# Optimization experiments

Measured on AMD Instinct MI355X. Metric: run time of the kernel, lower is better.

## Reference

```python
import jax, jax.numpy as jnp
import numpy as np

N_NODES = 100000
N_EDGES = 1600000
D_FEAT = 128


def setup_inputs() -> dict:
    key = jax.random.key(0)
    k1, k2, k3, k4 = jax.random.split(key, 4)
    support = jax.random.normal(k1, (N_NODES, D_FEAT), dtype=jnp.float32)
    vals = jax.random.uniform(k2, (N_EDGES,), dtype=jnp.float32)
    rows = jax.random.randint(k3, (N_EDGES,), 0, N_NODES, dtype=jnp.int64)
    cols = jax.random.randint(k4, (N_EDGES,), 0, N_NODES, dtype=jnp.int64)
    return {"support": support, "vals": vals, "rows": rows, "cols": cols}


def reference(support, vals, rows, cols):
    # out = adj @ support, adj given in COO: adj[rows[e], cols[e]] = vals[e]
    # Gather neighbor features, scale by edge weight, scatter-add to row nodes.
    msgs = vals[:, None] * support[cols]          # [E, F]
    out = jax.ops.segment_sum(msgs, rows, num_segments=support.shape[0])  # [N, F]
    return out
```

## Files before the change

### kernel.cpp

```cpp
#include <hip/hip_runtime.h>
#include <hip/hip_bf16.h>
#include <hip/hip_fp16.h>


#define D_FEAT 128
#define F4 32
#define H4 32
#define H8 16
#define STRIDE 64
#define OVF_CAP 131072
#define EPT 8
#define BINT 512
#define CAP 4096
#define GMAXIT 8
#define BROWS 200
#define GT 512

typedef float    vfloat4 __attribute__((ext_vector_type(4)));
typedef _Float16 half4v  __attribute__((ext_vector_type(4)));
typedef _Float16 half8v  __attribute__((ext_vector_type(8)));


__global__ __launch_bounds__(BINT) void
phase1_bin_kernel(const float4* __restrict__ support4,
                  half8v* __restrict__ supporth,
                  const int* __restrict__ rows,
                  const int* __restrict__ cols,
                  const float* __restrict__ vals,
                  int2* __restrict__ dense,
                  int* __restrict__ gcur,
                  int4* __restrict__ ovf,
                  int* __restrict__ ovf_count,
                  int E, int BT, int NBLK, int n8) {
    int b = blockIdx.x;
    int tid = threadIdx.x;

    if (b >= NBLK) {
        int m = (b - NBLK) * BINT + tid;
        if (m < n8) {
            float4 a0 = support4[(size_t)m * 2];
            float4 a1 = support4[(size_t)m * 2 + 1];
            half8v h;
            h[0] = (_Float16)a0.x; h[1] = (_Float16)a0.y;
            h[2] = (_Float16)a0.z; h[3] = (_Float16)a0.w;
            h[4] = (_Float16)a1.x; h[5] = (_Float16)a1.y;
            h[6] = (_Float16)a1.z; h[7] = (_Float16)a1.w;
            supporth[m] = h;
        }
        return;
    }

    __shared__ int  hist[512];
    __shared__ int  off[513];
    __shared__ int  sstart[512];
    __shared__ int2 sorted[BINT * EPT];

    for (int i = tid; i < 512; i += BINT) hist[i] = 0;
    __syncthreads();

    int t = b * BINT + tid;
    int   r[EPT];
    int   c[EPT];
    float v[EPT];
    int   rk[EPT];

    #pragma unroll
    for (int i = 0; i < EPT; ++i) {
        int e = t + i * BT;
        r[i] = (e < E) ? rows[e] : -1;
    }
    #pragma unroll
    for (int i = 0; i < EPT; ++i) {
        int e = t + i * BT;
        if (e < E) { c[i] = cols[e]; v[i] = vals[e]; }
    }
    #pragma unroll
    for (int i = 0; i < EPT; ++i)
        rk[i] = (r[i] >= 0) ? atomicAdd(&hist[r[i] / BROWS], 1) : 0;
    __syncthreads();

    if (tid < 64) {
        int l[8];
        int s = 0;
        #pragma unroll
        for (int k = 0; k < 8; ++k) {
            l[k] = hist[tid * 8 + k];
            s += l[k];
        }
        int inc = s;
        #pragma unroll
        for (int dd = 1; dd < 64; dd <<= 1) {
            int tt = __shfl_up(inc, dd, 64);
            if (tid >= dd) inc += tt;
        }
        int run = inc - s;
        #pragma unroll
        for (int k = 0; k < 8; ++k) {
            off[tid * 8 + k] = run;
            run += l[k];
        }
        if (tid == 63) off[512] = run;
    }
    __syncthreads();

    #pragma unroll
    for (int i = 0; i < EPT; ++i) {
        if (r[i] < 0) continue;
        int d = r[i] / BROWS;
        int2 q;
        q.x = ((r[i] - d * BROWS) << 17) | c[i];
        q.y = __float_as_int(v[i]);
        sorted[off[d] + rk[i]] = q;
    }
    __syncthreads();

    {
        int l = off[tid + 1] - off[tid];
        sstart[tid] = (l > 0) ? atomicAdd(&gcur[tid], l) : 0;
    }
    __syncthreads();

    {
        int grp  = tid >> 4;
        int lane = tid & 15;
        for (int d = grp; d < 512; d += 32) {
            int o  = off[d];
            int l  = off[d + 1] - o;
            int st = sstart[d];
            for (int k = lane; k < l; k += 16) {
                int pos = st + k;
                int2 q = sorted[o + k];
                if (pos < CAP) {
                    dense[(size_t)d * CAP + pos] = q;
                } else {
                    int ox = atomicAdd(ovf_count, 1);
                    if (ox < OVF_CAP) {
                        int4 e4;
                        e4.x = d * BROWS + ((q.x >> 17) & 255);
                        e4.y = q.x & 0x1FFFF;
                        e4.z = q.y;
                        e4.w = 0;
                        ovf[ox] = e4;
                    }
                }
            }
        }
    }
}


__global__ __launch_bounds__(GT) void
bucket_csr_gather_kernel(const half8v* __restrict__ supporth,
                         const int2* __restrict__ dense,
                         const int* __restrict__ gcur,
                         float4* __restrict__ out4, int N) {
    __shared__ int  cnt[257];
    __shared__ int  off[257];
    __shared__ int2 csr[CAP + 8];

    const int d   = blockIdx.x;
    const int tid = threadIdx.x;
    const int2* dbase = dense + (size_t)d * CAP;

    int total = gcur[d];
    if (total > CAP) total = CAP;

    if (tid < 257) cnt[tid] = 0;
    __syncthreads();

    int2 ent[GMAXIT];
    int  err[GMAXIT];
    int  ernk[GMAXIT];
    #pragma unroll
    for (int it = 0; it < GMAXIT; ++it) {
        int s = tid + it * GT;
        err[it] = -1;
        if (s < total) {
            int2 q = dbase[s];
            int r = (q.x >> 17) & 255;
            ent[it].x = q.x & 0x1FFFF;
            ent[it].y = q.y;
            err[it] = r;
            ernk[it] = atomicAdd(&cnt[r], 1);
        }
    }
    __syncthreads();

    if (tid < 64) {
        int4 c4 = ((int4*)cnt)[tid];
        int t0 = c4.x;
        int t1 = t0 + c4.y;
        int t2 = t1 + c4.z;
        int t3 = t2 + c4.w;
        int inc = t3;
        #pragma unroll
        for (int dd = 1; dd < 64; dd <<= 1) {
            int t = __shfl_up(inc, dd, 64);
            if (tid >= dd) inc += t;
        }
        int excl = inc - t3;
        off[tid * 4 + 0] = excl;
        off[tid * 4 + 1] = excl + t0;
        off[tid * 4 + 2] = excl + t1;
        off[tid * 4 + 3] = excl + t2;
        if (tid == 63) off[256] = inc;
    }
    __syncthreads();

    #pragma unroll
    for (int it = 0; it < GMAXIT; ++it) {
        if (err[it] >= 0)
            csr[off[err[it]] + ernk[it]] = ent[it];
    }
    __syncthreads();

    const int g = tid >> 4;
    const int i = tid & 15;
    const int base = d * BROWS;
    for (int rq = 0; rq < 7; ++rq) {
        int r = rq * 32 + g;
        if (r >= BROWS) continue;
        int beg = off[r];
        int end = off[r + 1];
        vfloat4 a00 = {0.f,0.f,0.f,0.f}, a01 = {0.f,0.f,0.f,0.f};
        vfloat4 a10 = {0.f,0.f,0.f,0.f}, a11 = {0.f,0.f,0.f,0.f};
        for (int k0 = beg; k0 < end; k0 += 8) {
            int   cc[8];
            float vv[8];
            #pragma unroll
            for (int u = 0; u < 8; ++u) {
                int2 e = csr[k0 + u];
                bool ib = (k0 + u) < end;
                cc[u] = ib ? e.x : 0;
                vv[u] = ib ? __int_as_float(e.y) : 0.f;
            }
            half8v s[8];
            #pragma unroll
            for (int u = 0; u < 8; ++u)
                s[u] = supporth[(size_t)cc[u] * H8 + i];
            #pragma unroll
            for (int u = 0; u < 8; ++u) {
                float v = vv[u];
                if (u & 1) {
                    a10.x += v * (float)s[u][0];
                    a10.y += v * (float)s[u][1];
                    a10.z += v * (float)s[u][2];
                    a10.w += v * (float)s[u][3];
                    a11.x += v * (float)s[u][4];
                    a11.y += v * (float)s[u][5];
                    a11.z += v * (float)s[u][6];
                    a11.w += v * (float)s[u][7];
                } else {
                    a00.x += v * (float)s[u][0];
                    a00.y += v * (float)s[u][1];
                    a00.z += v * (float)s[u][2];
                    a00.w += v * (float)s[u][3];
                    a01.x += v * (float)s[u][4];
                    a01.y += v * (float)s[u][5];
                    a01.z += v * (float)s[u][6];
                    a01.w += v * (float)s[u][7];
                }
            }
        }
        int row = base + r;
        if (row < N) {
            vfloat4 r0, r1;
            r0.x = a00.x + a10.x; r0.y = a00.y + a10.y;
            r0.z = a00.z + a10.z; r0.w = a00.w + a10.w;
            r1.x = a01.x + a11.x; r1.y = a01.y + a11.y;
            r1.z = a01.z + a11.z; r1.w = a01.w + a11.w;
            float4* dst = &out4[(size_t)row * F4 + (i << 1)];
            __builtin_nontemporal_store(r0, (vfloat4*)dst);
            __builtin_nontemporal_store(r1, (vfloat4*)(dst + 1));
        }
    }
}


__global__ void ovf_scatter_kernel(const float* __restrict__ support,
                                   const int4* __restrict__ ovf,
                                   const int* __restrict__ ovf_count,
                                   float* __restrict__ out, int cap) {
    int gid = blockIdx.x * blockDim.x + threadIdx.x;
    int i = gid >> 5;
    int j = gid & 31;
    int istride = (gridDim.x * blockDim.x) >> 5;
    int cnt = *ovf_count;
    if (cnt > cap) cnt = cap;
    for (; i < cnt; i += istride) {
        int4 q = ovf[i];
        float v = __int_as_float(q.z);
        const float4* s4 = (const float4*)support + (size_t)q.y * F4 + j;
        float4 s = *s4;
        float* o = out + (size_t)q.x * D_FEAT + j * 4;
        unsafeAtomicAdd(o + 0, v * s.x);
        unsafeAtomicAdd(o + 1, v * s.y);
        unsafeAtomicAdd(o + 2, v * s.z);
        unsafeAtomicAdd(o + 3, v * s.w);
    }
}


__global__ void convert_kernel(const float4* __restrict__ in,
                               half8v* __restrict__ out, int n8) {
    int t = blockIdx.x * blockDim.x + threadIdx.x;
    if (t >= n8) return;
    float4 a = in[(size_t)t * 2];
    float4 b = in[(size_t)t * 2 + 1];
    half8v h;
    h[0] = (_Float16)a.x; h[1] = (_Float16)a.y;
    h[2] = (_Float16)a.z; h[3] = (_Float16)a.w;
    h[4] = (_Float16)b.x; h[5] = (_Float16)b.y;
    h[6] = (_Float16)b.z; h[7] = (_Float16)b.w;
    out[t] = h;
}

__global__ void gather_half_kernel(const half4v* __restrict__ supporth,
                                   const int* __restrict__ cursor,
                                   const int2* __restrict__ pairs,
                                   float4* __restrict__ out4, int n_nodes) {
    unsigned int t = blockIdx.x * blockDim.x + threadIdx.x;
    unsigned int row = t >> 5;
    unsigned int j = t & 31;
    if (row >= (unsigned int)n_nodes) return;
    int deg = cursor[row];
    if (deg > STRIDE) deg = STRIDE;
    const int2* pr = pairs + (size_t)row * STRIDE;
    int2 z = {0, 0};
    int2 p0 = ((int)j < deg) ? pr[j] : z;
    int2 p1 = ((int)(j + 32) < deg) ? pr[j + 32] : z;
    int   c0 = p0.x;  float v0 = __int_as_float(p0.y);
    int   c1 = p1.x;  float v1 = __int_as_float(p1.y);
    int degr = (deg + 7) & ~7;
    float4 acc[4];
    #pragma unroll
    for (int u = 0; u < 4; ++u) acc[u] = {0.f, 0.f, 0.f, 0.f};
    for (int k = 0; k < degr; k += 8) {
        int   cc[8];
        float vv[8];
        #pragma unroll
        for (int u = 0; u < 8; ++u) {
            int kk = k + u;
            cc[u] = __shfl(kk < 32 ? c0 : c1, kk & 31, 32);
            vv[u] = __shfl(kk < 32 ? v0 : v1, kk & 31, 32);
        }
        half4v s[8];
        #pragma unroll
        for (int u = 0; u < 8; ++u)
            s[u] = supporth[(size_t)cc[u] * H4 + j];
        #pragma unroll
        for (int u = 0; u < 8; ++u) {
            acc[u & 3].x += vv[u] * (float)s[u][0];
            acc[u & 3].y += vv[u] * (float)s[u][1];
            acc[u & 3].z += vv[u] * (float)s[u][2];
            acc[u & 3].w += vv[u] * (float)s[u][3];
        }
    }
    vfloat4 res;
    res.x = (acc[0].x + acc[1].x) + (acc[2].x + acc[3].x);
    res.y = (acc[0].y + acc[1].y) + (acc[2].y + acc[3].y);
    res.z = (acc[0].z + acc[1].z) + (acc[2].z + acc[3].z);
    res.w = (acc[0].w + acc[1].w) + (acc[2].w + acc[3].w);
    __builtin_nontemporal_store(res, (vfloat4*)&out4[(size_t)row * F4 + j]);
}

__global__ void bucket_ilp_kernel(const int* __restrict__ rows,
                                  const int* __restrict__ cols,
                                  const float* __restrict__ vals,
                                  int* __restrict__ cursor,
                                  int* __restrict__ ovf_count,
                                  int2* __restrict__ pairs,
                                  int4* __restrict__ ovf,
                                  int n_edges, int gstride) {
    int tid = blockIdx.x * blockDim.x + threadIdx.x;
    int   r[EPT];
    int   c[EPT];
    float v[EPT];
    int   slot[EPT];
    #pragma unroll
    for (int i = 0; i < EPT; ++i) {
        int e = tid + i * gstride;
        r[i] = (e < n_edges) ? rows[e] : -1;
    }
    #pragma unroll
    for (int i = 0; i < EPT; ++i) {
        int e = tid + i * gstride;
        if (e < n_edges) { c[i] = cols[e]; v[i] = vals[e]; }
    }
    #pragma unroll
    for (int i = 0; i < EPT; ++i)
        slot[i] = (r[i] >= 0) ? atomicAdd(&cursor[r[i]], 1) : 0;
    #pragma unroll
    for (int i = 0; i < EPT; ++i) {
        if (r[i] < 0) continue;
        int2 p;
        p.x = c[i];
        p.y = __float_as_int(v[i]);
        if (slot[i] < STRIDE) {
            pairs[(size_t)r[i] * STRIDE + slot[i]] = p;
        } else {
            int o = atomicAdd(ovf_count, 1);
            if (o < OVF_CAP) {
                int4 q; q.x = r[i]; q.y = p.x; q.z = p.y; q.w = 0;
                ovf[o] = q;
            }
        }
    }
}


__global__ void gc_scatter_kernel(const float* __restrict__ support,
                                  const float* __restrict__ vals,
                                  const int* __restrict__ rows,
                                  const int* __restrict__ cols,
                                  float* __restrict__ out, int n_edges) {
    unsigned int t = blockIdx.x * blockDim.x + threadIdx.x;
    unsigned int e = t >> 5;
    unsigned int j = t & 31;
    if (e >= (unsigned int)n_edges) return;
    int r = rows[e];
    int c = cols[e];
    float v = vals[e];
    const float4* s4 = reinterpret_cast<const float4*>(support) + (size_t)c * F4 + j;
    float4 s = *s4;
    float* o = out + (size_t)r * D_FEAT + j * 4;
    unsafeAtomicAdd(o + 0, v * s.x);
    unsafeAtomicAdd(o + 1, v * s.y);
    unsafeAtomicAdd(o + 2, v * s.z);
    unsafeAtomicAdd(o + 3, v * s.w);
}


extern "C" void kernel_launch(void* const* d_in, const int* in_sizes, int n_in,
                              void* d_out, int out_size, void* d_ws, size_t ws_size,
                              hipStream_t stream) {
    const float* support = (const float*)d_in[0];
    const float* vals    = (const float*)d_in[1];
    const int*   rows    = (const int*)d_in[2];
    const int*   cols    = (const int*)d_in[3];
    float* out = (float*)d_out;

    int E = in_sizes[1];
    int N = in_sizes[0] / D_FEAT;
    int n8 = N * D_FEAT / 8;
    int ND = (N + BROWS - 1) / BROWS;
    int NBLK = (E + BINT * EPT - 1) / (BINT * EPT);
    int BT = NBLK * BINT;

    char* ws = (char*)d_ws;
    size_t cur = 0;
    auto carve = [&](size_t bytes) -> void* {
        void* p = ws + cur;
        cur += (bytes + 255) & ~(size_t)255;
        return p;
    };

    {
        size_t save = cur;
        int2*   dense     = (int2*)carve((size_t)512 * CAP * 8);
        int*    gcur      = (int*)carve((size_t)768 * 4);
        int4*   ovf       = (int4*)carve((size_t)OVF_CAP * 16);
        half8v* supporth  = (half8v*)carve((size_t)N * D_FEAT * 2);
        if (cur <= ws_size && ND <= 512) {
            int* ovf_count = gcur + 512;
            (void)hipMemsetAsync(gcur, 0, (size_t)513 * 4, stream);
            int cblocks = (n8 + BINT - 1) / BINT;
            phase1_bin_kernel<<<NBLK + cblocks, BINT, 0, stream>>>(
                (const float4*)support, supporth, rows, cols, vals,
                dense, gcur, ovf, ovf_count, E, BT, NBLK, n8);
            bucket_csr_gather_kernel<<<ND, GT, 0, stream>>>(
                supporth, dense, gcur, (float4*)out, N);
            ovf_scatter_kernel<<<128, 256, 0, stream>>>(
                support, ovf, ovf_count, out, OVF_CAP);
            return;
        }
        cur = save;
    }

    {
        size_t save = cur;
        int*    cursor   = (int*)carve((size_t)(N + 1) * 4);
        int2*   pairs    = (int2*)carve((size_t)N * STRIDE * 8);
        int4*   ovf      = (int4*)carve((size_t)8192 * 16);
        half8v* supporth = (half8v*)carve((size_t)N * D_FEAT * 2);
        if (cur <= ws_size) {
            int* ovf_count = cursor + N;
            int bthreads = (E + EPT - 1) / EPT;
            int bblocks = (bthreads + 255) / 256;
            int gstride = bblocks * 256;
            (void)hipMemsetAsync(cursor, 0, (size_t)(N + 1) * 4, stream);
            convert_kernel<<<(n8 + 255) / 256, 256, 0, stream>>>(
                (const float4*)support, supporth, n8);
            bucket_ilp_kernel<<<bblocks, 256, 0, stream>>>(
                rows, cols, vals, cursor, ovf_count, pairs, ovf, E, gstride);
            unsigned int gthreads = (unsigned int)N * 32;
            gather_half_kernel<<<(gthreads + 255) / 256, 256, 0, stream>>>(
                (const half4v*)supporth, cursor, pairs, (float4*)out, N);
            ovf_scatter_kernel<<<512, 256, 0, stream>>>(
                support, ovf, ovf_count, out, 8192);
            return;
        }
        cur = save;
    }

    (void)hipMemsetAsync(d_out, 0, (size_t)out_size * sizeof(float), stream);
    unsigned int total = (unsigned int)E * 32;
    gc_scatter_kernel<<<(total + 255) / 256, 256, 0, stream>>>(
        support, vals, rows, cols, out, E);
}
```

Measured before the change: 185.0 us.

## Use finer row buckets and fold overflow edges into bucket gather kernel

Halves rows per bucket (100) and doubles bucket count to 1024, with 1024-thread binning blocks and a smaller per-bucket capacity, so the gather kernel launches about 1000 blocks instead of about 500 for better occupancy. The separate overflow scatter kernel is removed. Each gather block now scans the global overflow list and inserts its own rows' overflow entries into its shared CSR. This drops a launch and atomic scatter work, but every block rereads the whole overflow list, and the 1024-thread binning block needs 64KB of shared sorted buffer, which may limit occupancy.

```diff
diff --git a/kernel.cpp b/kernel.cpp
--- a/kernel.cpp
+++ b/kernel.cpp
@@ -10,11 +10,13 @@
 #define STRIDE 64
 #define OVF_CAP 131072
 #define EPT 8
-#define BINT 512
-#define CAP 4096
-#define GMAXIT 8
-#define BROWS 200
+#define BINT 1024
+#define NBINS 1024
+#define CAP 2048
+#define GMAXIT 4
+#define BROWS 100
 #define GT 512
+#define CSRCAP (CAP + 64)
 
 typedef float    vfloat4 __attribute__((ext_vector_type(4)));
 typedef _Float16 half4v  __attribute__((ext_vector_type(4)));
@@ -50,12 +52,12 @@
         return;
     }
 
-    __shared__ int  hist[512];
-    __shared__ int  off[513];
-    __shared__ int  sstart[512];
+    __shared__ int  hist[NBINS];
+    __shared__ int  off[NBINS + 1];
+    __shared__ int  sstart[NBINS];
     __shared__ int2 sorted[BINT * EPT];
 
-    for (int i = tid; i < 512; i += BINT) hist[i] = 0;
+    for (int i = tid; i < NBINS; i += BINT) hist[i] = 0;
     __syncthreads();
 
     int t = b * BINT + tid;
@@ -80,11 +82,11 @@
     __syncthreads();
 
     if (tid < 64) {
-        int l[8];
+        int l[16];
         int s = 0;
         #pragma unroll
-        for (int k = 0; k < 8; ++k) {
-            l[k] = hist[tid * 8 + k];
+        for (int k = 0; k < 16; ++k) {
+            l[k] = hist[tid * 16 + k];
             s += l[k];
         }
         int inc = s;
@@ -95,11 +97,11 @@
         }
         int run = inc - s;
         #pragma unroll
-        for (int k = 0; k < 8; ++k) {
-            off[tid * 8 + k] = run;
+        for (int k = 0; k < 16; ++k) {
+            off[tid * 16 + k] = run;
             run += l[k];
         }
-        if (tid == 63) off[512] = run;
+        if (tid == 63) off[NBINS] = run;
     }
     __syncthreads();
 
@@ -123,7 +125,7 @@
     {
         int grp  = tid >> 4;
         int lane = tid & 15;
-        for (int d = grp; d < 512; d += 32) {
+        for (int d = grp; d < NBINS; d += 64) {
             int o  = off[d];
             int l  = off[d + 1] - o;
             int st = sstart[d];
@@ -153,19 +155,26 @@
 bucket_csr_gather_kernel(const half8v* __restrict__ supporth,
                          const int2* __restrict__ dense,
                          const int* __restrict__ gcur,
+                         const int4* __restrict__ ovf,
+                         const int* __restrict__ ovf_count,
                          float4* __restrict__ out4, int N) {
-    __shared__ int  cnt[257];
-    __shared__ int  off[257];
-    __shared__ int2 csr[CAP + 8];
+    __shared__ __align__(16) int cnt[128];
+    __shared__ __align__(16) int oc[128];
+    __shared__ int oc2[128];
+    __shared__ int off[129];
+    __shared__ int2 csr[CSRCAP + 8];
 
     const int d   = blockIdx.x;
     const int tid = threadIdx.x;
     const int2* dbase = dense + (size_t)d * CAP;
+    const int base = d * BROWS;
 
     int total = gcur[d];
     if (total > CAP) total = CAP;
-
-    if (tid < 257) cnt[tid] = 0;
+    int ocnt = *ovf_count;
+    if (ocnt > OVF_CAP) ocnt = OVF_CAP;
+
+    if (tid < 128) { cnt[tid] = 0; oc[tid] = 0; oc2[tid] = 0; }
     __syncthreads();
 
     int2 ent[GMAXIT];
@@ -184,18 +193,25 @@
             ernk[it] = atomicAdd(&cnt[r], 1);
         }
     }
-    __syncthreads();
-
-    if (tid < 64) {
+    if (ocnt > 0) {
+        for (int i = tid; i < ocnt; i += GT) {
+            int rr = ovf[i].x - base;
+            if (rr >= 0 && rr < BROWS) atomicAdd(&oc[rr], 1);
+        }
+    }
+    __syncthreads();
+
+    if (tid < 32) {
         int4 c4 = ((int4*)cnt)[tid];
-        int t0 = c4.x;
-        int t1 = t0 + c4.y;
-        int t2 = t1 + c4.z;
-        int t3 = t2 + c4.w;
+        int4 o4 = ((int4*)oc)[tid];
+        int t0 = c4.x + o4.x;
+        int t1 = t0 + c4.y + o4.y;
+        int t2 = t1 + c4.z + o4.z;
+        int t3 = t2 + c4.w + o4.w;
         int inc = t3;
         #pragma unroll
-        for (int dd = 1; dd < 64; dd <<= 1) {
-            int t = __shfl_up(inc, dd, 64);
+        for (int dd = 1; dd < 32; dd <<= 1) {
+            int t = __shfl_up(inc, dd, 32);
             if (tid >= dd) inc += t;
         }
         int excl = inc - t3;
@@ -203,7 +219,7 @@
         off[tid * 4 + 1] = excl + t0;
         off[tid * 4 + 2] = excl + t1;
         off[tid * 4 + 3] = excl + t2;
-        if (tid == 63) off[256] = inc;
+        if (tid == 31) off[128] = inc;
     }
     __syncthreads();
 
@@ -212,12 +228,21 @@
         if (err[it] >= 0)
             csr[off[err[it]] + ernk[it]] = ent[it];
     }
+    if (ocnt > 0) {
+        for (int i = tid; i < ocnt; i += GT) {
+            int4 q = ovf[i];
+            int rr = q.x - base;
+            if (rr >= 0 && rr < BROWS) {
+                int idx = off[rr] + cnt[rr] + atomicAdd(&oc2[rr], 1);
+                if (idx < CSRCAP) { int2 e; e.x = q.y; e.y = q.z; csr[idx] = e; }
+            }
+        }
+    }
     __syncthreads();
 
     const int g = tid >> 4;
     const int i = tid & 15;
-    const int base = d * BROWS;
-    for (int rq = 0; rq < 7; ++rq) {
+    for (int rq = 0; rq < 4; ++rq) {
         int r = rq * 32 + g;
         if (r >= BROWS) continue;
         int beg = off[r];
@@ -457,21 +482,19 @@
 
     {
         size_t save = cur;
-        int2*   dense     = (int2*)carve((size_t)512 * CAP * 8);
-        int*    gcur      = (int*)carve((size_t)768 * 4);
+        int2*   dense     = (int2*)carve((size_t)NBINS * CAP * 8);
+        int*    gcur      = (int*)carve((size_t)(NBINS + 256) * 4);
         int4*   ovf       = (int4*)carve((size_t)OVF_CAP * 16);
         half8v* supporth  = (half8v*)carve((size_t)N * D_FEAT * 2);
-        if (cur <= ws_size && ND <= 512) {
-            int* ovf_count = gcur + 512;
-            (void)hipMemsetAsync(gcur, 0, (size_t)513 * 4, stream);
+        if (cur <= ws_size && ND <= NBINS) {
+            int* ovf_count = gcur + NBINS;
+            (void)hipMemsetAsync(gcur, 0, (size_t)(NBINS + 1) * 4, stream);
             int cblocks = (n8 + BINT - 1) / BINT;
             phase1_bin_kernel<<<NBLK + cblocks, BINT, 0, stream>>>(
                 (const float4*)support, supporth, rows, cols, vals,
                 dense, gcur, ovf, ovf_count, E, BT, NBLK, n8);
             bucket_csr_gather_kernel<<<ND, GT, 0, stream>>>(
-                supporth, dense, gcur, (float4*)out, N);
-            ovf_scatter_kernel<<<128, 256, 0, stream>>>(
-                support, ovf, ovf_count, out, OVF_CAP);
+                supporth, dense, gcur, ovf, ovf_count, (float4*)out, N);
             return;
         }
         cur = save;
```

New measurement: 180.4 us. 2.5% less time.
